# Performance work log

Measured on AMD Instinct MI355X. Metric: run time of the kernel, lower is better.

The kernel has to match this reference:

```python
import jax, jax.numpy as jnp
import numpy as np

IN_CH, C_M, C_N = 512, 512, 128
B, H, W = 16, 56, 56


def setup_inputs() -> dict:
    key = jax.random.key(0)
    ks = jax.random.split(key, 7)
    s = 1.0 / np.sqrt(IN_CH)
    return {
        "x": jax.random.normal(ks[0], (B, IN_CH, H, W), dtype=jnp.float32),
        "wA": jax.random.uniform(ks[1], (C_M, IN_CH), jnp.float32, -s, s),
        "bA": jax.random.uniform(ks[2], (C_M,), jnp.float32, -s, s),
        "wB": jax.random.uniform(ks[3], (C_N, IN_CH), jnp.float32, -s, s),
        "bB": jax.random.uniform(ks[4], (C_N,), jnp.float32, -s, s),
        "wV": jax.random.uniform(ks[5], (C_N, IN_CH), jnp.float32, -s, s),
        "bV": jax.random.uniform(ks[6], (C_N,), jnp.float32, -s, s),
        "K": 1,
    }


def reference(x, wA, bA, wB, bB, wV, bV, K):
    b, c, h, w = x.shape
    c_m, c_n = wA.shape[0], wB.shape[0]
    batch = b // K
    hw = h * w
    N = K * hw
    # 1x1 convs == channel-wise matmuls
    A = jnp.einsum('bchw,mc->bmhw', x, wA) + bA[None, :, None, None]
    Bf = jnp.einsum('bchw,nc->bnhw', x, wB) + bB[None, :, None, None]
    Vf = jnp.einsum('bchw,nc->bnhw', x, wV) + bV[None, :, None, None]
    # (batch, c_m, K*h*w)
    tmpA = A.reshape(batch, K, c_m, hw).transpose(0, 2, 1, 3).reshape(batch, c_m, N)
    # softmax over the spatial dim N (torch Softmax() on 2D -> dim=1)
    tmpB = Bf.reshape(batch, K, c_n, hw).transpose(0, 2, 1, 3).reshape(batch, c_n, N)
    attB = jax.nn.softmax(tmpB, axis=-1).transpose(0, 2, 1)  # (batch, N, c_n)
    # softmax over channel dim c_n
    tmpV = Vf.reshape(batch, K, c_n, hw).transpose(0, 1, 3, 2).reshape(batch, N, c_n)
    attV = jax.nn.softmax(tmpV, axis=-1).transpose(0, 2, 1)  # (batch, c_n, N)
    G = jnp.matmul(tmpA, attB)   # (batch, c_m, c_n) global descriptors
    Z = jnp.matmul(G, attV)      # (batch, c_m, N) distribute
    Z = Z.reshape(batch, c_m, K, hw).transpose(0, 2, 1, 3).reshape(b, c_m, h, w)
    return Z
```

## Files before the change

### kernel.cpp

```cpp
#include <hip/hip_runtime.h>
#include <hip/hip_bf16.h>

#define BATCH 16
#define CIN   512
#define HW    3136
#define CM    512
#define CN    128

typedef short short8 __attribute__((ext_vector_type(8)));
typedef float f32x4  __attribute__((ext_vector_type(4)));

#define MFMA(a,b,c) __builtin_amdgcn_mfma_f32_16x16x32_bf16((a),(b),(c),0,0,0)

__device__ __forceinline__ void cvt_store8(__bf16* dst, const float* src) {
  const f32x4 a = *(const f32x4*)src;
  const f32x4 b = *(const f32x4*)(src + 4);
  __attribute__((aligned(16))) __bf16 t[8];
  t[0] = (__bf16)a[0]; t[1] = (__bf16)a[1]; t[2] = (__bf16)a[2]; t[3] = (__bf16)a[3];
  t[4] = (__bf16)b[0]; t[5] = (__bf16)b[1]; t[6] = (__bf16)b[2]; t[7] = (__bf16)b[3];
  *(uint4*)dst = *(uint4*)t;
}

__global__ __launch_bounds__(256) void conv_bv_kernel(
    const float* __restrict__ x,
    const float* __restrict__ wB, const float* __restrict__ wV,
    const float* __restrict__ bB, const float* __restrict__ bV,
    __bf16* __restrict__ BVB, __bf16* __restrict__ attVT,
    float* __restrict__ bsum)
{
  const int s0  = blockIdx.x * 64;
  const int b   = blockIdx.y;
  const int tid = threadIdx.x;
  const int lane = tid & 63, w = tid >> 6;
  const int l15  = lane & 15, q = lane >> 4;

  __shared__ __attribute__((aligned(16))) char smem[46080];
  __bf16* Wt = (__bf16*)smem;
  __bf16* Xt = (__bf16*)(smem + 36864);
  __bf16* T  = (__bf16*)smem;
  __shared__ float Vm[2][64];
  __shared__ float Vs[2][64];

  f32x4 acc[4][4] = {};
  const float* xb = x + (size_t)b*CIN*HW + s0;
  const int colg = tid & 7, row0 = tid >> 3;
  const int cl = 2*(tid >> 3);

  for (int k0 = 0; k0 < CIN; k0 += 64) {
    #pragma unroll
    for (int p = 0; p < 8; ++p) {
      int row = row0 + 32*p;
      const float* src = (row < 128) ? (wB + row*512) : (wV + (row-128)*512);
      cvt_store8(&Wt[row*72 + colg*8], src + k0 + colg*8);
    }
    {
      const float* r0 = xb + (size_t)(k0 + cl)*HW + colg*8;
      const float* r1 = r0 + HW;
      f32x4 a0 = *(const f32x4*)r0, a1 = *(const f32x4*)(r0 + 4);
      f32x4 b0 = *(const f32x4*)r1, b1 = *(const f32x4*)(r1 + 4);
      float va[8] = {a0[0],a0[1],a0[2],a0[3],a1[0],a1[1],a1[2],a1[3]};
      float vb[8] = {b0[0],b0[1],b0[2],b0[3],b1[0],b1[1],b1[2],b1[3]};
      const int off = ((cl >> 3) ^ colg)*8 + (cl & 7);
      #pragma unroll
      for (int j = 0; j < 8; ++j) {
        int s = colg*8 + j;
        __attribute__((aligned(4))) __bf16 pairv[2] = { (__bf16)va[j], (__bf16)vb[j] };
        *(unsigned int*)&Xt[s*72 + off] = *(unsigned int*)pairv;
      }
    }
    __syncthreads();
    #pragma unroll
    for (int kk = 0; kk < 2; ++kk) {
      short8 a[4], bb[4];
      #pragma unroll
      for (int mi = 0; mi < 4; ++mi)
        a[mi] = *(short8*)&Wt[(w*64 + mi*16 + l15)*72 + kk*32 + q*8];
      #pragma unroll
      for (int si = 0; si < 4; ++si) {
        int s = si*16 + l15;
        int oct = (kk*4 + q) ^ (si*2 + (l15 >> 3));
        bb[si] = *(short8*)&Xt[s*72 + oct*8];
      }
      #pragma unroll
      for (int mi = 0; mi < 4; ++mi)
        #pragma unroll
        for (int si = 0; si < 4; ++si)
          acc[mi][si] = MFMA(a[mi], bb[si], acc[mi][si]);
    }
    __syncthreads();
  }

  float bias[4][4];
  #pragma unroll
  for (int mi = 0; mi < 4; ++mi)
    #pragma unroll
    for (int r = 0; r < 4; ++r) {
      int nch = w*64 + mi*16 + q*4 + r;
      bias[mi][r] = (nch < CN) ? bB[nch] : bV[nch - CN];
    }

  if (w < 2) {
    const size_t outb = (size_t)b * CN * HW;
    float psum[4][4] = {};
    #pragma unroll
    for (int mi = 0; mi < 4; ++mi)
      #pragma unroll
      for (int si = 0; si < 4; ++si) {
        int s = s0 + si*16 + l15;
        #pragma unroll
        for (int r = 0; r < 4; ++r) {
          int nch = w*64 + mi*16 + q*4 + r;
          __bf16 bv = (__bf16)(acc[mi][si][r] + bias[mi][r]);
          BVB[outb + (size_t)nch*HW + s] = bv;
          psum[mi][r] += __expf((float)bv);
        }
      }
    #pragma unroll
    for (int mi = 0; mi < 4; ++mi)
      #pragma unroll
      for (int r = 0; r < 4; ++r) {
        float v = psum[mi][r];
        v += __shfl_xor(v, 1); v += __shfl_xor(v, 2);
        v += __shfl_xor(v, 4); v += __shfl_xor(v, 8);
        if (l15 == 0) {
          int nch = w*64 + mi*16 + q*4 + r;
          atomicAdd(&bsum[b*CN + nch], v);
        }
      }
  } else {
    #pragma unroll
    for (int si = 0; si < 4; ++si) {
      float m = -1e30f;
      #pragma unroll
      for (int mi = 0; mi < 4; ++mi)
        #pragma unroll
        for (int r = 0; r < 4; ++r)
          m = fmaxf(m, acc[mi][si][r] + bias[mi][r]);
      m = fmaxf(m, __shfl_xor(m, 16));
      m = fmaxf(m, __shfl_xor(m, 32));
      if (q == 0) Vm[w-2][si*16 + l15] = m;
    }
  }
  __syncthreads();
  if (w >= 2) {
    #pragma unroll
    for (int si = 0; si < 4; ++si) {
      int idx = si*16 + l15;
      float ms = fmaxf(Vm[0][idx], Vm[1][idx]);
      float ssum = 0.f;
      #pragma unroll
      for (int mi = 0; mi < 4; ++mi)
        #pragma unroll
        for (int r = 0; r < 4; ++r) {
          float e = __expf(acc[mi][si][r] + bias[mi][r] - ms);
          acc[mi][si][r] = e;
          ssum += e;
        }
      ssum += __shfl_xor(ssum, 16);
      ssum += __shfl_xor(ssum, 32);
      if (q == 0) Vs[w-2][idx] = ssum;
    }
  }
  __syncthreads();
  if (w >= 2) {
    #pragma unroll
    for (int si = 0; si < 4; ++si) {
      int idx = si*16 + l15;
      float inv = 1.0f / (Vs[0][idx] + Vs[1][idx]);
      #pragma unroll
      for (int mi = 0; mi < 4; ++mi)
        #pragma unroll
        for (int r = 0; r < 4; ++r) {
          int j = (w-2)*64 + mi*16 + q*4 + r;
          T[idx*136 + j] = (__bf16)(acc[mi][si][r] * inv);
        }
    }
  }
  __syncthreads();
  __bf16* dst = attVT + ((size_t)b*HW + s0)*CN;
  #pragma unroll
  for (int k = 0; k < 4; ++k) {
    int chunk = tid + 256*k;
    int row = chunk >> 4, oct = chunk & 15;
    *(uint4*)&dst[(size_t)row*CN + oct*8] = *(uint4*)&T[row*136 + oct*8];
  }
}

__global__ __launch_bounds__(256) void h_gemm_kernel(
    const float* __restrict__ x, const __bf16* __restrict__ BVB,
    const float* __restrict__ bsum, float* __restrict__ H)
{
  const int c0 = blockIdx.x * 128, b = blockIdx.y, kc = blockIdx.z;
  const int tid = threadIdx.x, lane = tid & 63, w = tid >> 6;
  const int l15 = lane & 15, q = lane >> 4;

  __shared__ __attribute__((aligned(16))) __bf16 At[128*72];
  __shared__ __attribute__((aligned(16))) __bf16 Bt[128*72];
  f32x4 acc[8][2] = {};

  const float* xb = x + ((size_t)b*CIN + c0)*HW;
  const __bf16* ab = BVB + (size_t)b*CN*HW;
  const float* bsb = bsum + b*CN;
  const int colg = tid & 7, row0 = tid >> 3;

  float irow[4];
  #pragma unroll
  for (int p = 0; p < 4; ++p) irow[p] = 1.0f / bsb[row0 + 32*p];

  for (int ki = 0; ki < 7; ++ki) {
    int k0 = kc*448 + ki*64;
    #pragma unroll
    for (int p = 0; p < 4; ++p) {
      int row = row0 + 32*p;
      cvt_store8(&At[row*72 + colg*8], xb + (size_t)row*HW + k0 + colg*8);
    }
    #pragma unroll
    for (int p = 0; p < 4; ++p) {
      int row = row0 + 32*p;
      uint4 rawv = *(const uint4*)(ab + (size_t)row*HW + k0 + colg*8);
      const __bf16* v = (const __bf16*)&rawv;
      __attribute__((aligned(16))) __bf16 t[8];
      #pragma unroll
      for (int j = 0; j < 8; ++j)
        t[j] = (__bf16)(__expf((float)v[j]) * irow[p]);
      *(uint4*)&Bt[row*72 + colg*8] = *(uint4*)t;
    }
    __syncthreads();
    #pragma unroll
    for (int kk = 0; kk < 2; ++kk) {
      short8 a[8], bb[2];
      #pragma unroll
      for (int mi = 0; mi < 8; ++mi)
        a[mi] = *(short8*)&At[(mi*16 + l15)*72 + kk*32 + q*8];
      #pragma unroll
      for (int ni = 0; ni < 2; ++ni)
        bb[ni] = *(short8*)&Bt[(w*32 + ni*16 + l15)*72 + kk*32 + q*8];
      #pragma unroll
      for (int mi = 0; mi < 8; ++mi)
        #pragma unroll
        for (int ni = 0; ni < 2; ++ni)
          acc[mi][ni] = MFMA(a[mi], bb[ni], acc[mi][ni]);
    }
    __syncthreads();
  }

  float* Hb = H + (size_t)b*CIN*CN;
  #pragma unroll
  for (int mi = 0; mi < 8; ++mi)
    #pragma unroll
    for (int ni = 0; ni < 2; ++ni)
      #pragma unroll
      for (int r = 0; r < 4; ++r) {
        int c = c0 + mi*16 + q*4 + r;
        int n = w*32 + ni*16 + l15;
        atomicAdd(&Hb[c*CN + n], acc[mi][ni][r]);
      }
}

__global__ __launch_bounds__(256) void g_gemm_kernel(
    const float* __restrict__ wA, const float* __restrict__ bA,
    const float* __restrict__ H, __bf16* __restrict__ G)
{
  const int m0 = blockIdx.x * 64, b = blockIdx.y;
  const int tid = threadIdx.x, lane = tid & 63, w = tid >> 6;
  const int l15 = lane & 15, q = lane >> 4;

  __shared__ __attribute__((aligned(16))) __bf16 At[64*72];
  __shared__ __attribute__((aligned(16))) __bf16 Bt[128*72];
  f32x4 acc[4][2] = {};

  const float* Hb = H + (size_t)b*CIN*CN;
  const int colg = tid & 7, row0 = tid >> 3;
  const int nn = tid & 127, gh = tid >> 7;

  for (int k0 = 0; k0 < CIN; k0 += 64) {
    #pragma unroll
    for (int p = 0; p < 2; ++p) {
      int row = row0 + 32*p;
      cvt_store8(&At[row*72 + colg*8], wA + (size_t)(m0+row)*CIN + k0 + colg*8);
    }
    #pragma unroll
    for (int p = 0; p < 4; ++p) {
      int g = gh + 2*p;
      __attribute__((aligned(16))) __bf16 tmp[8];
      #pragma unroll
      for (int j = 0; j < 8; ++j)
        tmp[j] = (__bf16)Hb[(size_t)(k0 + g*8 + j)*CN + nn];
      *(uint4*)&Bt[nn*72 + g*8] = *(uint4*)tmp;
    }
    __syncthreads();
    #pragma unroll
    for (int kk = 0; kk < 2; ++kk) {
      short8 a[4], bb[2];
      #pragma unroll
      for (int mi = 0; mi < 4; ++mi)
        a[mi] = *(short8*)&At[(mi*16 + l15)*72 + kk*32 + q*8];
      #pragma unroll
      for (int ni = 0; ni < 2; ++ni)
        bb[ni] = *(short8*)&Bt[(w*32 + ni*16 + l15)*72 + kk*32 + q*8];
      #pragma unroll
      for (int mi = 0; mi < 4; ++mi)
        #pragma unroll
        for (int ni = 0; ni < 2; ++ni)
          acc[mi][ni] = MFMA(a[mi], bb[ni], acc[mi][ni]);
    }
    __syncthreads();
  }

  #pragma unroll
  for (int mi = 0; mi < 4; ++mi)
    #pragma unroll
    for (int ni = 0; ni < 2; ++ni)
      #pragma unroll
      for (int r = 0; r < 4; ++r) {
        int m = m0 + mi*16 + q*4 + r;
        int n = w*32 + ni*16 + l15;
        G[((size_t)b*CM + m)*CN + n] = (__bf16)(acc[mi][ni][r] + bA[m]);
      }
}

__global__ __launch_bounds__(256) void z_gemm_kernel(
    const __bf16* __restrict__ G, const __bf16* __restrict__ attVT,
    float* __restrict__ out)
{
  const int m0 = blockIdx.x * 128, s0 = blockIdx.y * 64, b = blockIdx.z;
  const int tid = threadIdx.x, lane = tid & 63, w = tid >> 6;
  const int l15 = lane & 15, q = lane >> 4;

  __shared__ __attribute__((aligned(16))) __bf16 At[128*136];
  __shared__ __attribute__((aligned(16))) __bf16 Bt[64*136];

  const __bf16* Gb = G + ((size_t)b*CM + m0)*CN;
  const __bf16* Vb = attVT + ((size_t)b*HW + s0)*CN;
  const int g = tid & 15, r0 = tid >> 4;
  #pragma unroll
  for (int p = 0; p < 8; ++p) {
    int row = r0 + 16*p;
    *(uint4*)&At[row*136 + g*8] = *(const uint4*)(Gb + (size_t)row*CN + g*8);
  }
  #pragma unroll
  for (int p = 0; p < 4; ++p) {
    int row = r0 + 16*p;
    *(uint4*)&Bt[row*136 + g*8] = *(const uint4*)(Vb + (size_t)row*CN + g*8);
  }
  __syncthreads();

  f32x4 acc[8] = {};
  #pragma unroll
  for (int kk = 0; kk < 4; ++kk) {
    short8 bb = *(short8*)&Bt[(w*16 + l15)*136 + kk*32 + q*8];
    #pragma unroll
    for (int mi = 0; mi < 8; ++mi) {
      short8 a = *(short8*)&At[(mi*16 + l15)*136 + kk*32 + q*8];
      acc[mi] = MFMA(a, bb, acc[mi]);
    }
  }

  const int s = s0 + w*16 + l15;
  #pragma unroll
  for (int mi = 0; mi < 8; ++mi)
    #pragma unroll
    for (int r = 0; r < 4; ++r) {
      int m = m0 + mi*16 + q*4 + r;
      out[((size_t)b*CM + m)*HW + s] = acc[mi][r];
    }
}

extern "C" void kernel_launch(void* const* d_in, const int* in_sizes, int n_in,
                              void* d_out, int out_size, void* d_ws, size_t ws_size,
                              hipStream_t stream)
{
  (void)in_sizes; (void)n_in; (void)out_size; (void)ws_size;
  const float* x  = (const float*)d_in[0];
  const float* wA = (const float*)d_in[1];
  const float* bA = (const float*)d_in[2];
  const float* wB = (const float*)d_in[3];
  const float* bB = (const float*)d_in[4];
  const float* wV = (const float*)d_in[5];
  const float* bV = (const float*)d_in[6];
  float* out = (float*)d_out;

  char* ws = (char*)d_ws;
  const size_t szBVB   = (size_t)BATCH*CN*HW*2;
  const size_t szAttVT = (size_t)BATCH*HW*CN*2;
  const size_t szH     = (size_t)BATCH*CIN*CN*4;
  const size_t szBsum  = (size_t)BATCH*CN*4;

  char* p = ws;
  __bf16* BVB   = (__bf16*)p; p += szBVB;
  __bf16* attVT = (__bf16*)p; p += szAttVT;
  float*  H     = (float*)p;  p += szH;
  float*  bsum  = (float*)p;  p += szBsum;
  __bf16* G     = (__bf16*)p;

  hipMemsetAsync(H, 0, szH + szBsum, stream);
  conv_bv_kernel<<<dim3(49,16),   256, 0, stream>>>(x, wB, wV, bB, bV, BVB, attVT, bsum);
  h_gemm_kernel <<<dim3(4,16,7),  256, 0, stream>>>(x, BVB, bsum, H);
  g_gemm_kernel <<<dim3(8,16),    256, 0, stream>>>(wA, bA, H, G);
  z_gemm_kernel <<<dim3(4,49,16), 256, 0, stream>>>(G, attVT, out);
}
```

Before: 298.5 us.

## Pre-convert B/V weights to padded bf16 image, async-load to LDS, prefetch x

Adds a small prep kernel that converts wB and wV to bf16 once per call, laid out in the padded per-k-tile LDS format. conv_bv then copies each weight tile straight into shared memory with global_load_lds instead of having every block reload fp32 weights and convert them. It also register-prefetches the next k-tile of x while the current tile is staged, to overlap global latency with compute. The cost is an extra kernel launch and a workspace buffer, and the code assumes the workspace holds the extra weight image.

```diff
diff --git a/kernel.cpp b/kernel.cpp
--- a/kernel.cpp
+++ b/kernel.cpp
@@ -21,9 +21,30 @@
   *(uint4*)dst = *(uint4*)t;
 }
 
+__device__ __forceinline__ void load_lds16(const void* g, void* l) {
+  __builtin_amdgcn_global_load_lds(
+      (const __attribute__((address_space(1))) unsigned int*)g,
+      (__attribute__((address_space(3))) unsigned int*)l, 16, 0, 0);
+}
+
+__global__ __launch_bounds__(256) void prep_w_kernel(
+    const float* __restrict__ wB, const float* __restrict__ wV,
+    __bf16* __restrict__ Wimg)
+{
+  const int k0  = blockIdx.x >> 2;
+  const int row = (blockIdx.x & 3) * 64 + (threadIdx.x >> 2);
+  const int c0  = (threadIdx.x & 3) * 16;
+  const float* src = (row < 128) ? (wB + (size_t)row * CIN)
+                                 : (wV + (size_t)(row - 128) * CIN);
+  src += k0 * 64 + c0;
+  __bf16* dst = Wimg + (size_t)k0 * 18432 + row * 72 + c0;
+  cvt_store8(dst, src);
+  cvt_store8(dst + 8, src + 8);
+}
+
 __global__ __launch_bounds__(256) void conv_bv_kernel(
     const float* __restrict__ x,
-    const float* __restrict__ wB, const float* __restrict__ wV,
+    const __bf16* __restrict__ Wimg,
     const float* __restrict__ bB, const float* __restrict__ bV,
     __bf16* __restrict__ BVB, __bf16* __restrict__ attVT,
     float* __restrict__ bsum)
@@ -43,30 +64,41 @@
 
   f32x4 acc[4][4] = {};
   const float* xb = x + (size_t)b*CIN*HW + s0;
-  const int colg = tid & 7, row0 = tid >> 3;
+  const int colg = tid & 7;
   const int cl = 2*(tid >> 3);
+  const int xoff = ((cl >> 3) ^ colg)*8 + (cl & 7);
+
+  f32x4 pa0, pa1, pb0, pb1;
+  {
+    const float* r0 = xb + (size_t)cl*HW + colg*8;
+    const float* r1 = r0 + HW;
+    pa0 = *(const f32x4*)r0; pa1 = *(const f32x4*)(r0 + 4);
+    pb0 = *(const f32x4*)r1; pb1 = *(const f32x4*)(r1 + 4);
+  }
 
   for (int k0 = 0; k0 < CIN; k0 += 64) {
-    #pragma unroll
-    for (int p = 0; p < 8; ++p) {
-      int row = row0 + 32*p;
-      const float* src = (row < 128) ? (wB + row*512) : (wV + (row-128)*512);
-      cvt_store8(&Wt[row*72 + colg*8], src + k0 + colg*8);
-    }
     {
-      const float* r0 = xb + (size_t)(k0 + cl)*HW + colg*8;
-      const float* r1 = r0 + HW;
-      f32x4 a0 = *(const f32x4*)r0, a1 = *(const f32x4*)(r0 + 4);
-      f32x4 b0 = *(const f32x4*)r1, b1 = *(const f32x4*)(r1 + 4);
-      float va[8] = {a0[0],a0[1],a0[2],a0[3],a1[0],a1[1],a1[2],a1[3]};
-      float vb[8] = {b0[0],b0[1],b0[2],b0[3],b1[0],b1[1],b1[2],b1[3]};
-      const int off = ((cl >> 3) ^ colg)*8 + (cl & 7);
+      float va[8] = {pa0[0],pa0[1],pa0[2],pa0[3],pa1[0],pa1[1],pa1[2],pa1[3]};
+      float vb[8] = {pb0[0],pb0[1],pb0[2],pb0[3],pb1[0],pb1[1],pb1[2],pb1[3]};
       #pragma unroll
       for (int j = 0; j < 8; ++j) {
         int s = colg*8 + j;
         __attribute__((aligned(4))) __bf16 pairv[2] = { (__bf16)va[j], (__bf16)vb[j] };
-        *(unsigned int*)&Xt[s*72 + off] = *(unsigned int*)pairv;
-      }
+        *(unsigned int*)&Xt[s*72 + xoff] = *(unsigned int*)pairv;
+      }
+    }
+    {
+      const char* wsrc = (const char*)Wimg + (size_t)(k0 >> 6)*36864 + tid*16;
+      char* wdst = (char*)Wt + tid*16;
+      #pragma unroll
+      for (int i = 0; i < 9; ++i)
+        load_lds16(wsrc + i*4096, wdst + i*4096);
+    }
+    if (k0 + 64 < CIN) {
+      const float* r0 = xb + (size_t)(k0 + 64 + cl)*HW + colg*8;
+      const float* r1 = r0 + HW;
+      pa0 = *(const f32x4*)r0; pa1 = *(const f32x4*)(r0 + 4);
+      pb0 = *(const f32x4*)r1; pb1 = *(const f32x4*)(r1 + 4);
     }
     __syncthreads();
     #pragma unroll
@@ -385,16 +417,19 @@
   const size_t szAttVT = (size_t)BATCH*HW*CN*2;
   const size_t szH     = (size_t)BATCH*CIN*CN*4;
   const size_t szBsum  = (size_t)BATCH*CN*4;
+  const size_t szG     = (size_t)BATCH*CM*CN*2;
 
   char* p = ws;
   __bf16* BVB   = (__bf16*)p; p += szBVB;
   __bf16* attVT = (__bf16*)p; p += szAttVT;
   float*  H     = (float*)p;  p += szH;
   float*  bsum  = (float*)p;  p += szBsum;
-  __bf16* G     = (__bf16*)p;
+  __bf16* G     = (__bf16*)p; p += szG;
+  __bf16* Wimg  = (__bf16*)p;
 
   hipMemsetAsync(H, 0, szH + szBsum, stream);
-  conv_bv_kernel<<<dim3(49,16),   256, 0, stream>>>(x, wB, wV, bB, bV, BVB, attVT, bsum);
+  prep_w_kernel <<<dim3(32),      256, 0, stream>>>(wB, wV, Wimg);
+  conv_bv_kernel<<<dim3(49,16),   256, 0, stream>>>(x, Wimg, bB, bV, BVB, attVT, bsum);
   h_gemm_kernel <<<dim3(4,16,7),  256, 0, stream>>>(x, BVB, bsum, H);
   g_gemm_kernel <<<dim3(8,16),    256, 0, stream>>>(wA, bA, H, G);
   z_gemm_kernel <<<dim3(4,49,16), 256, 0, stream>>>(G, attVT, out);
```

Result: faster. 283.8 us (-4.9%).

## Pre-swizzle bf16 operand images and load MFMA fragments directly from global

Applied to the files above, without the earlier changes.

Adds prep kernels that convert the conv weights and x into bf16 images laid out in MFMA fragment order. The conv, H-GEMM and Z-GEMM kernels now load fragments straight from global memory into registers with double buffering instead of staging through LDS, and the LDS syncthreads are replaced with lighter lgkmcnt-plus-barrier calls. This removes LDS round trips and barriers from the main loops. In exchange it adds two extra launches and an extra bf16 copy of x written and read back, and it relies on global-load latency being hidden by the register prefetch.

```diff
diff --git a/kernel.cpp b/kernel.cpp
--- a/kernel.cpp
+++ b/kernel.cpp
@@ -11,6 +11,12 @@
 typedef float f32x4  __attribute__((ext_vector_type(4)));
 
 #define MFMA(a,b,c) __builtin_amdgcn_mfma_f32_16x16x32_bf16((a),(b),(c),0,0,0)
+
+__device__ __forceinline__ void wg_barrier() {
+  asm volatile("s_waitcnt lgkmcnt(0)" ::: "memory");
+  __builtin_amdgcn_s_barrier();
+  asm volatile("" ::: "memory");
+}
 
 __device__ __forceinline__ void cvt_store8(__bf16* dst, const float* src) {
   const f32x4 a = *(const f32x4*)src;
@@ -21,9 +27,63 @@
   *(uint4*)dst = *(uint4*)t;
 }
 
+__device__ __forceinline__ short8 cvt_frag(f32x4 a, f32x4 b) {
+  union { __bf16 h[8]; short8 s; } u;
+  u.h[0] = (__bf16)a[0]; u.h[1] = (__bf16)a[1]; u.h[2] = (__bf16)a[2]; u.h[3] = (__bf16)a[3];
+  u.h[4] = (__bf16)b[0]; u.h[5] = (__bf16)b[1]; u.h[6] = (__bf16)b[2]; u.h[7] = (__bf16)b[3];
+  return u.s;
+}
+
+__global__ __launch_bounds__(256) void prep_w_kernel(
+    const float* __restrict__ wB, const float* __restrict__ wV,
+    __bf16* __restrict__ Wimg)
+{
+  const int gid  = blockIdx.x * 256 + threadIdx.x;
+  const int lane = gid & 63;
+  const int kk   = (gid >> 6) & 1;
+  const int mi   = (gid >> 7) & 3;
+  const int w    = (gid >> 9) & 3;
+  const int st   = (gid >> 11) & 7;
+  const int row  = w*64 + mi*16 + (lane & 15);
+  const int col  = st*64 + kk*32 + (lane >> 4)*8;
+  const float* src = (row < 128) ? (wB + (size_t)row * CIN)
+                                 : (wV + (size_t)(row - 128) * CIN);
+  cvt_store8(Wimg + (size_t)gid * 8, src + col);
+}
+
+__global__ __launch_bounds__(256) void prep_x_kernel(
+    const float* __restrict__ x, __bf16* __restrict__ Ximg)
+{
+  const int sx = blockIdx.x, st = blockIdx.y, b = blockIdx.z;
+  const int s0 = sx*64, c0 = st*64;
+  const int tid = threadIdx.x;
+  __shared__ __attribute__((aligned(16))) __bf16 Lp[64*80];
+
+  {
+    const int c_l = tid >> 2, s_q = tid & 3;
+    const float* src = x + ((size_t)(b*CIN + c0 + c_l))*HW + s0 + s_q*16;
+    cvt_store8(&Lp[c_l*80 + s_q*16], src);
+    cvt_store8(&Lp[c_l*80 + s_q*16 + 8], src + 8);
+  }
+  __syncthreads();
+  __bf16* img = Ximg + (((size_t)b*49 + sx)*8 + st)*4096;
+  #pragma unroll
+  for (int r = 0; r < 2; ++r) {
+    const int ch = tid + 256*r;
+    const int lane = ch & 63, si2kk = ch >> 6;
+    const int si = si2kk >> 1, kk = si2kk & 1;
+    const int qq = lane >> 4, ll = lane & 15;
+    const int s_l = si*16 + ll;
+    const int cb = (kk*4 + qq)*8;
+    __attribute__((aligned(16))) __bf16 t[8];
+    #pragma unroll
+    for (int j = 0; j < 8; ++j) t[j] = Lp[(cb + j)*80 + s_l];
+    *(uint4*)&img[ch*8] = *(uint4*)t;
+  }
+}
+
 __global__ __launch_bounds__(256) void conv_bv_kernel(
-    const float* __restrict__ x,
-    const float* __restrict__ wB, const float* __restrict__ wV,
+    const __bf16* __restrict__ Ximg, const __bf16* __restrict__ Wimg,
     const float* __restrict__ bB, const float* __restrict__ bV,
     __bf16* __restrict__ BVB, __bf16* __restrict__ attVT,
     float* __restrict__ bsum)
@@ -34,61 +94,39 @@
   const int lane = tid & 63, w = tid >> 6;
   const int l15  = lane & 15, q = lane >> 4;
 
-  __shared__ __attribute__((aligned(16))) char smem[46080];
-  __bf16* Wt = (__bf16*)smem;
-  __bf16* Xt = (__bf16*)(smem + 36864);
-  __bf16* T  = (__bf16*)smem;
   __shared__ float Vm[2][64];
   __shared__ float Vs[2][64];
+  __shared__ __attribute__((aligned(16))) __bf16 T[64*136];
 
   f32x4 acc[4][4] = {};
-  const float* xb = x + (size_t)b*CIN*HW + s0;
-  const int colg = tid & 7, row0 = tid >> 3;
-  const int cl = 2*(tid >> 3);
-
-  for (int k0 = 0; k0 < CIN; k0 += 64) {
-    #pragma unroll
-    for (int p = 0; p < 8; ++p) {
-      int row = row0 + 32*p;
-      const float* src = (row < 128) ? (wB + row*512) : (wV + (row-128)*512);
-      cvt_store8(&Wt[row*72 + colg*8], src + k0 + colg*8);
-    }
-    {
-      const float* r0 = xb + (size_t)(k0 + cl)*HW + colg*8;
-      const float* r1 = r0 + HW;
-      f32x4 a0 = *(const f32x4*)r0, a1 = *(const f32x4*)(r0 + 4);
-      f32x4 b0 = *(const f32x4*)r1, b1 = *(const f32x4*)(r1 + 4);
-      float va[8] = {a0[0],a0[1],a0[2],a0[3],a1[0],a1[1],a1[2],a1[3]};
-      float vb[8] = {b0[0],b0[1],b0[2],b0[3],b1[0],b1[1],b1[2],b1[3]};
-      const int off = ((cl >> 3) ^ colg)*8 + (cl & 7);
-      #pragma unroll
-      for (int j = 0; j < 8; ++j) {
-        int s = colg*8 + j;
-        __attribute__((aligned(4))) __bf16 pairv[2] = { (__bf16)va[j], (__bf16)vb[j] };
-        *(unsigned int*)&Xt[s*72 + off] = *(unsigned int*)pairv;
-      }
-    }
-    __syncthreads();
-    #pragma unroll
-    for (int kk = 0; kk < 2; ++kk) {
-      short8 a[4], bb[4];
-      #pragma unroll
-      for (int mi = 0; mi < 4; ++mi)
-        a[mi] = *(short8*)&Wt[(w*64 + mi*16 + l15)*72 + kk*32 + q*8];
-      #pragma unroll
-      for (int si = 0; si < 4; ++si) {
-        int s = si*16 + l15;
-        int oct = (kk*4 + q) ^ (si*2 + (l15 >> 3));
-        bb[si] = *(short8*)&Xt[s*72 + oct*8];
-      }
+  const char* wb_ = (const char*)Wimg + (size_t)w*8192 + (size_t)lane*16;
+  const char* xb_ = (const char*)Ximg + ((size_t)b*49 + blockIdx.x)*65536
+                    + (size_t)lane*16;
+
+  short8 wf[2][8], xf[2][8];
+#define WLOAD(P, ST) do { const char* p_ = wb_ + (size_t)(ST)*32768; \
+    _Pragma("unroll") for (int i_ = 0; i_ < 8; ++i_) \
+      wf[P][i_] = *(const short8*)(p_ + i_*1024); } while(0)
+#define XLOAD(P, ST) do { const char* p_ = xb_ + (size_t)(ST)*8192; \
+    _Pragma("unroll") for (int i_ = 0; i_ < 8; ++i_) \
+      xf[P][i_] = *(const short8*)(p_ + i_*1024); } while(0)
+
+  WLOAD(0, 0);
+  XLOAD(0, 0);
+  #pragma unroll
+  for (int st = 0; st < 8; ++st) {
+    const int p = st & 1;
+    if (st < 7) { WLOAD(p^1, st+1); XLOAD(p^1, st+1); }
+    #pragma unroll
+    for (int kk = 0; kk < 2; ++kk)
       #pragma unroll
       for (int mi = 0; mi < 4; ++mi)
         #pragma unroll
         for (int si = 0; si < 4; ++si)
-          acc[mi][si] = MFMA(a[mi], bb[si], acc[mi][si]);
-    }
-    __syncthreads();
-  }
+          acc[mi][si] = MFMA(wf[p][mi*2+kk], xf[p][si*2+kk], acc[mi][si]);
+  }
+#undef WLOAD
+#undef XLOAD
 
   float bias[4][4];
   #pragma unroll
@@ -141,7 +179,7 @@
       if (q == 0) Vm[w-2][si*16 + l15] = m;
     }
   }
-  __syncthreads();
+  wg_barrier();
   if (w >= 2) {
     #pragma unroll
     for (int si = 0; si < 4; ++si) {
@@ -161,7 +199,7 @@
       if (q == 0) Vs[w-2][idx] = ssum;
     }
   }
-  __syncthreads();
+  wg_barrier();
   if (w >= 2) {
     #pragma unroll
     for (int si = 0; si < 4; ++si) {
@@ -176,7 +214,7 @@
         }
     }
   }
-  __syncthreads();
+  wg_barrier();
   __bf16* dst = attVT + ((size_t)b*HW + s0)*CN;
   #pragma unroll
   for (int k = 0; k < 4; ++k) {
@@ -193,66 +231,63 @@
   const int c0 = blockIdx.x * 128, b = blockIdx.y, kc = blockIdx.z;
   const int tid = threadIdx.x, lane = tid & 63, w = tid >> 6;
   const int l15 = lane & 15, q = lane >> 4;
-
-  __shared__ __attribute__((aligned(16))) __bf16 At[128*72];
-  __shared__ __attribute__((aligned(16))) __bf16 Bt[128*72];
-  f32x4 acc[8][2] = {};
-
-  const float* xb = x + ((size_t)b*CIN + c0)*HW;
-  const __bf16* ab = BVB + (size_t)b*CN*HW;
-  const float* bsb = bsum + b*CN;
-  const int colg = tid & 7, row0 = tid >> 3;
+  const int wm = (w >> 1) * 64;
+  const int wn = (w & 1) * 64;
+
+  f32x4 acc[4][4] = {};
+  const float*  xa = x   + ((size_t)(b*CIN + c0 + wm + l15))*HW + q*8;
+  const __bf16* bv = BVB + ((size_t)(b*CN  + wn + l15))*HW + q*8;
 
   float irow[4];
   #pragma unroll
-  for (int p = 0; p < 4; ++p) irow[p] = 1.0f / bsb[row0 + 32*p];
-
-  for (int ki = 0; ki < 7; ++ki) {
-    int k0 = kc*448 + ki*64;
-    #pragma unroll
-    for (int p = 0; p < 4; ++p) {
-      int row = row0 + 32*p;
-      cvt_store8(&At[row*72 + colg*8], xb + (size_t)row*HW + k0 + colg*8);
-    }
-    #pragma unroll
-    for (int p = 0; p < 4; ++p) {
-      int row = row0 + 32*p;
-      uint4 rawv = *(const uint4*)(ab + (size_t)row*HW + k0 + colg*8);
-      const __bf16* v = (const __bf16*)&rawv;
-      __attribute__((aligned(16))) __bf16 t[8];
+  for (int ni = 0; ni < 4; ++ni)
+    irow[ni] = 1.0f / bsum[b*CN + wn + ni*16 + l15];
+
+  const int kbase = kc * 448;
+  f32x4  pa[2][4][2];
+  short8 pb[2][4];
+#define HLOADA(P, K) do { _Pragma("unroll") for (int mi_ = 0; mi_ < 4; ++mi_) { \
+    const float* s_ = xa + (size_t)mi_*16*HW + (K); \
+    pa[P][mi_][0] = *(const f32x4*)s_; pa[P][mi_][1] = *(const f32x4*)(s_ + 4); } } while(0)
+#define HLOADB(P, K) do { _Pragma("unroll") for (int ni_ = 0; ni_ < 4; ++ni_) \
+    pb[P][ni_] = *(const short8*)(bv + (size_t)ni_*16*HW + (K)); } while(0)
+
+  HLOADA(0, kbase);
+  HLOADB(0, kbase);
+  #pragma unroll
+  for (int hs = 0; hs < 14; ++hs) {
+    const int p = hs & 1;
+    if (hs < 13) { HLOADA(p^1, kbase + (hs+1)*32); HLOADB(p^1, kbase + (hs+1)*32); }
+    short8 af[4], bf[4];
+    #pragma unroll
+    for (int mi = 0; mi < 4; ++mi) af[mi] = cvt_frag(pa[p][mi][0], pa[p][mi][1]);
+    #pragma unroll
+    for (int ni = 0; ni < 4; ++ni) {
+      const __bf16* vv = (const __bf16*)&pb[p][ni];
+      union { __bf16 h[8]; short8 s; } u;
       #pragma unroll
       for (int j = 0; j < 8; ++j)
-        t[j] = (__bf16)(__expf((float)v[j]) * irow[p]);
-      *(uint4*)&Bt[row*72 + colg*8] = *(uint4*)t;
-    }
-    __syncthreads();
-    #pragma unroll
-    for (int kk = 0; kk < 2; ++kk) {
-      short8 a[8], bb[2];
-      #pragma unroll
-      for (int mi = 0; mi < 8; ++mi)
-        a[mi] = *(short8*)&At[(mi*16 + l15)*72 + kk*32 + q*8];
-      #pragma unroll
-      for (int ni = 0; ni < 2; ++ni)
-        bb[ni] = *(short8*)&Bt[(w*32 + ni*16 + l15)*72 + kk*32 + q*8];
-      #pragma unroll
-      for (int mi = 0; mi < 8; ++mi)
-        #pragma unroll
-        for (int ni = 0; ni < 2; ++ni)
-          acc[mi][ni] = MFMA(a[mi], bb[ni], acc[mi][ni]);
-    }
-    __syncthreads();
-  }
+        u.h[j] = (__bf16)(__expf((float)vv[j]) * irow[ni]);
+      bf[ni] = u.s;
+    }
+    #pragma unroll
+    for (int mi = 0; mi < 4; ++mi)
+      #pragma unroll
+      for (int ni = 0; ni < 4; ++ni)
+        acc[mi][ni] = MFMA(af[mi], bf[ni], acc[mi][ni]);
+  }
+#undef HLOADA
+#undef HLOADB
 
   float* Hb = H + (size_t)b*CIN*CN;
   #pragma unroll
-  for (int mi = 0; mi < 8; ++mi)
-    #pragma unroll
-    for (int ni = 0; ni < 2; ++ni)
+  for (int mi = 0; mi < 4; ++mi)
+    #pragma unroll
+    for (int ni = 0; ni < 4; ++ni)
       #pragma unroll
       for (int r = 0; r < 4; ++r) {
-        int c = c0 + mi*16 + q*4 + r;
-        int n = w*32 + ni*16 + l15;
+        int c = c0 + wm + mi*16 + q*4 + r;
+        int n = wn + ni*16 + l15;
         atomicAdd(&Hb[c*CN + n], acc[mi][ni][r]);
       }
 }
@@ -288,7 +323,7 @@
         tmp[j] = (__bf16)Hb[(size_t)(k0 + g*8 + j)*CN + nn];
       *(uint4*)&Bt[nn*72 + g*8] = *(uint4*)tmp;
     }
-    __syncthreads();
+    wg_barrier();
     #pragma unroll
     for (int kk = 0; kk < 2; ++kk) {
       short8 a[4], bb[2];
@@ -304,7 +339,7 @@
         for (int ni = 0; ni < 2; ++ni)
           acc[mi][ni] = MFMA(a[mi], bb[ni], acc[mi][ni]);
     }
-    __syncthreads();
+    wg_barrier();
   }
 
   #pragma unroll
@@ -327,34 +362,29 @@
   const int tid = threadIdx.x, lane = tid & 63, w = tid >> 6;
   const int l15 = lane & 15, q = lane >> 4;
 
-  __shared__ __attribute__((aligned(16))) __bf16 At[128*136];
-  __shared__ __attribute__((aligned(16))) __bf16 Bt[64*136];
-
-  const __bf16* Gb = G + ((size_t)b*CM + m0)*CN;
-  const __bf16* Vb = attVT + ((size_t)b*HW + s0)*CN;
-  const int g = tid & 15, r0 = tid >> 4;
-  #pragma unroll
-  for (int p = 0; p < 8; ++p) {
-    int row = r0 + 16*p;
-    *(uint4*)&At[row*136 + g*8] = *(const uint4*)(Gb + (size_t)row*CN + g*8);
-  }
-  #pragma unroll
-  for (int p = 0; p < 4; ++p) {
-    int row = r0 + 16*p;
-    *(uint4*)&Bt[row*136 + g*8] = *(const uint4*)(Vb + (size_t)row*CN + g*8);
-  }
-  __syncthreads();
-
+  const __bf16* Ga = G + ((size_t)(b*CM + m0 + l15))*CN + q*8;
+  const __bf16* Va = attVT + ((size_t)(b*HW + s0 + w*16 + l15))*CN + q*8;
+
+  short8 bb[4];
+  #pragma unroll
+  for (int kk = 0; kk < 4; ++kk)
+    bb[kk] = *(const short8*)(Va + kk*32);
+
+  short8 a[2][8];
+#define ZLOADA(P, KK) do { _Pragma("unroll") for (int mi_ = 0; mi_ < 8; ++mi_) \
+    a[P][mi_] = *(const short8*)(Ga + (size_t)mi_*16*CN + (KK)*32); } while(0)
+
+  ZLOADA(0, 0);
   f32x4 acc[8] = {};
   #pragma unroll
   for (int kk = 0; kk < 4; ++kk) {
-    short8 bb = *(short8*)&Bt[(w*16 + l15)*136 + kk*32 + q*8];
-    #pragma unroll
-    for (int mi = 0; mi < 8; ++mi) {
-      short8 a = *(short8*)&At[(mi*16 + l15)*136 + kk*32 + q*8];
-      acc[mi] = MFMA(a, bb, acc[mi]);
-    }
-  }
+    const int p = kk & 1;
+    if (kk < 3) ZLOADA(p^1, kk+1);
+    #pragma unroll
+    for (int mi = 0; mi < 8; ++mi)
+      acc[mi] = MFMA(a[p][mi], bb[kk], acc[mi]);
+  }
+#undef ZLOADA
 
   const int s = s0 + w*16 + l15;
   #pragma unroll
@@ -385,17 +415,23 @@
   const size_t szAttVT = (size_t)BATCH*HW*CN*2;
   const size_t szH     = (size_t)BATCH*CIN*CN*4;
   const size_t szBsum  = (size_t)BATCH*CN*4;
+  const size_t szG     = (size_t)BATCH*CM*CN*2;
+  const size_t szWimg  = (size_t)16384*16;
 
   char* p = ws;
   __bf16* BVB   = (__bf16*)p; p += szBVB;
   __bf16* attVT = (__bf16*)p; p += szAttVT;
   float*  H     = (float*)p;  p += szH;
   float*  bsum  = (float*)p;  p += szBsum;
-  __bf16* G     = (__bf16*)p;
+  __bf16* G     = (__bf16*)p; p += szG;
+  __bf16* Wimg  = (__bf16*)p; p += szWimg;
+  __bf16* Ximg  = (__bf16*)p;
 
   hipMemsetAsync(H, 0, szH + szBsum, stream);
-  conv_bv_kernel<<<dim3(49,16),   256, 0, stream>>>(x, wB, wV, bB, bV, BVB, attVT, bsum);
-  h_gemm_kernel <<<dim3(4,16,7),  256, 0, stream>>>(x, BVB, bsum, H);
-  g_gemm_kernel <<<dim3(8,16),    256, 0, stream>>>(wA, bA, H, G);
-  z_gemm_kernel <<<dim3(4,49,16), 256, 0, stream>>>(G, attVT, out);
-}
+  prep_w_kernel <<<dim3(64),       256, 0, stream>>>(wB, wV, Wimg);
+  prep_x_kernel <<<dim3(49,8,16),  256, 0, stream>>>(x, Ximg);
+  conv_bv_kernel<<<dim3(49,16),    256, 0, stream>>>(Ximg, Wimg, bB, bV, BVB, attVT, bsum);
+  h_gemm_kernel <<<dim3(4,16,7),   256, 0, stream>>>(x, BVB, bsum, H);
+  g_gemm_kernel <<<dim3(8,16),     256, 0, stream>>>(wA, bA, H, G);
+  z_gemm_kernel <<<dim3(4,49,16),  256, 0, stream>>>(G, attVT, out);
+}
```

Measured after the change: 361.9 us. +21.2%, slower.
